# Optimization experiments

Measured on AMD Instinct MI355X. Metric: run time of the kernel, lower is better.

## Reference

```python
import jax, jax.numpy as jnp
import numpy as np

HEADS, DIM_HEAD, C, B, HS, WS = 8, 64, 512, 2, 48, 48


def setup_inputs() -> dict:
    key = jax.random.key(0)
    ks = jax.random.split(key, 9)
    s = 0.02
    return {
        "hidden_states": jax.random.normal(ks[0], (B, C, HS, WS), jnp.float32),
        "Wq": jax.random.normal(ks[1], (HEADS, DIM_HEAD, C), jnp.float32) * s,
        "bq": jax.random.normal(ks[2], (HEADS, DIM_HEAD), jnp.float32) * s,
        "Wk": jax.random.normal(ks[3], (HEADS, DIM_HEAD, C), jnp.float32) * s,
        "bk": jax.random.normal(ks[4], (HEADS, DIM_HEAD), jnp.float32) * s,
        "Wv": jax.random.normal(ks[5], (HEADS, DIM_HEAD, C), jnp.float32) * s,
        "bv": jax.random.normal(ks[6], (HEADS, DIM_HEAD), jnp.float32) * s,
        "Wo": jax.random.normal(ks[7], (C, HEADS * DIM_HEAD), jnp.float32) * s,
        "bo": jax.random.normal(ks[8], (C,), jnp.float32) * s,
    }


def reference(hidden_states, Wq, bq, Wk, bk, Wv, bv, Wo, bo):
    # hidden_states: [B, C, H, W]; per-head 1x1 convs == per-head linear over C.
    b, c, h, w = hidden_states.shape
    hw = h * w
    x = hidden_states.reshape(b, c, hw)  # [B, C, HW]
    # Batched per-head projections (fuses the per-head Conv2d loop).
    q = jnp.einsum('bcs,ndc->bnsd', x, Wq) + bq[None, :, None, :]  # [B, n, HW, d]
    k = jnp.einsum('bcs,ndc->bnsd', x, Wk) + bk[None, :, None, :]
    v = jnp.einsum('bcs,ndc->bnsd', x, Wv) + bv[None, :, None, :]
    scale = 1.0 / jnp.sqrt(jnp.asarray(DIM_HEAD, hidden_states.dtype))
    scores = jnp.einsum('bnqd,bnkd->bnqk', q, k) * scale  # [B, n, HW, HW]
    probs = jax.nn.softmax(scores, axis=-1)
    attn = jnp.einsum('bnqk,bnkd->bnqd', probs, v)  # [B, n, HW, d]
    # concat heads along last dim (matches torch.cat(..., dim=-1))
    attn = attn.transpose(0, 2, 1, 3).reshape(b, hw, HEADS * DIM_HEAD)
    out = attn @ Wo.T + bo  # [B, HW, C] (to_out[0]; to_out[1] dropout = identity)
    out = out.reshape(b, h, w, c).transpose(0, 3, 1, 2)  # [B, C, H, W]
    return out
```

## Files before the change

### kernel.cpp

```cpp
#include <hip/hip_runtime.h>
#include <hip/hip_bf16.h>

#define HEADS 8
#define DHEAD 64
#define CDIM  512
#define SEQ   2304
#define ND    512
#define NCHUNK 4

typedef unsigned short u16;
typedef unsigned int   u32;
typedef __attribute__((ext_vector_type(8))) short short8;
typedef __attribute__((ext_vector_type(4))) float f32x4;

#define QSCALE 0.18033688011112043f

__device__ __forceinline__ u16 f2bf(float f) {
    union { float f; u32 u; } x; x.f = f;
    u32 r = x.u + 0x7FFFu + ((x.u >> 16) & 1u);
    return (u16)(r >> 16);
}
__device__ __forceinline__ float bf2f(u16 v) {
    union { u32 u; float f; } x; x.u = ((u32)v) << 16; return x.f;
}
__device__ __forceinline__ u32 pkbf(float a, float b) {
    union { float f; u32 u; } x, y; x.f = a; y.f = b;
    return __builtin_amdgcn_perm(y.u + 0x8000u, x.u + 0x8000u, 0x07060302u);
}
__device__ __forceinline__ u32 cvtpk(float lo, float hi) {
    u32 r;
    asm("v_cvt_pk_bf16_f32 %0, %1, %2" : "=v"(r) : "v"(lo), "v"(hi));
    return r;
}
__device__ __forceinline__ f32x4 mfma16(short8 a, short8 b, f32x4 c) {
    return __builtin_amdgcn_mfma_f32_16x16x32_bf16(a, b, c, 0, 0, 0);
}
__device__ __forceinline__ void cp16(const void* g, void* l) {
    __builtin_amdgcn_global_load_lds(
        (const __attribute__((address_space(1))) u32*)(uintptr_t)g,
        (__attribute__((address_space(3))) u32*)(u32)(uintptr_t)l,
        16, 0, 0);
}
__device__ __forceinline__ int kperm_inv(int r) {
    return (r & ~0x1C) | ((r & 0x0C) << 1) | ((r & 0x10) >> 2);
}

__global__ void prep_kernel(const float* __restrict__ H,
                            const float* __restrict__ Wq, const float* __restrict__ Wk,
                            const float* __restrict__ Wv, const float* __restrict__ Wo,
                            u16* __restrict__ Wqkv, u16* __restrict__ Wob,
                            u16* __restrict__ X) {
    __shared__ float tile[32][33];
    const int t = threadIdx.x;
    const int bx = blockIdx.x;
    if (bx < 512) {
        const int N1 = CDIM * ND;
        int i8 = (bx * 256 + t) * 8;
        const float* src;
        u16* dst;
        if (i8 < 3 * N1) {
            src = (i8 < N1) ? &Wq[i8] : (i8 < 2 * N1 ? &Wk[i8 - N1] : &Wv[i8 - 2 * N1]);
            dst = &Wqkv[i8];
        } else {
            src = &Wo[i8 - 3 * N1];
            dst = &Wob[i8 - 3 * N1];
        }
        float4 a = *(const float4*)src;
        float4 c = *(const float4*)(src + 4);
        uint4 o;
        o.x = pkbf(a.x, a.y); o.y = pkbf(a.z, a.w);
        o.z = pkbf(c.x, c.y); o.w = pkbf(c.z, c.w);
        *(uint4*)dst = o;
    } else {
        int bb = bx - 512;
        int st = bb % 72, ct = (bb / 72) % 16, b = bb / (72 * 16);
        int cl = t >> 3, j4 = (t & 7) * 4;
        float4 hv = *(const float4*)&H[((size_t)b * CDIM + ct * 32 + cl) * SEQ + st * 32 + j4];
        tile[cl][j4 + 0] = hv.x; tile[cl][j4 + 1] = hv.y;
        tile[cl][j4 + 2] = hv.z; tile[cl][j4 + 3] = hv.w;
        __syncthreads();
        int sl = t >> 3, c4 = (t & 7) * 4;
        uint2 ov;
        ov.x = cvtpk(tile[c4 + 0][sl], tile[c4 + 1][sl]);
        ov.y = cvtpk(tile[c4 + 2][sl], tile[c4 + 3][sl]);
        *(uint2*)&X[((size_t)b * SEQ + st * 32 + sl) * CDIM + ct * 32 + c4] = ov;
    }
}

__global__ __launch_bounds__(256) void gemm_qkv_kernel(
        const u16* __restrict__ W, const u16* __restrict__ X,
        const float* __restrict__ bq, const float* __restrict__ bk, const float* __restrict__ bv,
        u16* __restrict__ Q, u16* __restrict__ K, u16* __restrict__ V) {
    __shared__ __align__(16) u16 sm[2 * (64 * 64 + 128 * 64)];
    const int n0 = blockIdx.x * 128;
    const int m0 = blockIdx.y * 64;
    const int b  = blockIdx.z;
    const int t = threadIdx.x;
    const int lane = t & 63, w = t >> 6;
    const int l16 = lane & 15, quad = lane >> 4;
    const int x7 = l16 & 7;
    const int srow = t >> 3, scol = (t & 7) * 8;
    const int scol_sw = ((t & 7) ^ (srow & 7)) * 8;
    const u16* Xb = X + (size_t)b * SEQ * CDIM;

    f32x4 acc[4][2] = {};

    {
        u16* As = sm; u16* Bs = sm + 4096;
#pragma unroll
        for (int it = 0; it < 2; ++it) {
            int r2 = it * 32 + srow;
            cp16(&W[(size_t)(m0 + r2) * 512 + scol_sw], &As[r2 * 64 + scol]);
        }
#pragma unroll
        for (int it = 0; it < 4; ++it) {
            int r2 = it * 32 + srow;
            cp16(&Xb[(size_t)(n0 + r2) * 512 + scol_sw], &Bs[r2 * 64 + scol]);
        }
    }
    for (int kb = 0; kb < 512; kb += 64) {
        const int pb = (kb >> 6) & 1;
        const u16* As = sm + pb * 12288;
        const u16* Bs = As + 4096;
        __syncthreads();
        if (kb + 64 < 512) {
            u16* An = sm + (pb ^ 1) * 12288;
            u16* Bn = An + 4096;
#pragma unroll
            for (int it = 0; it < 2; ++it) {
                int r2 = it * 32 + srow;
                cp16(&W[(size_t)(m0 + r2) * 512 + kb + 64 + scol_sw], &An[r2 * 64 + scol]);
            }
#pragma unroll
            for (int it = 0; it < 4; ++it) {
                int r2 = it * 32 + srow;
                cp16(&Xb[(size_t)(n0 + r2) * 512 + kb + 64 + scol_sw], &Bn[r2 * 64 + scol]);
            }
        }
#pragma unroll
        for (int kk = 0; kk < 2; ++kk) {
            const int co = ((kk * 4 + quad) ^ x7) * 8;
            short8 af[4], bfr[2];
#pragma unroll
            for (int i = 0; i < 4; ++i)
                af[i] = *(const short8*)&As[(i * 16 + l16) * 64 + co];
#pragma unroll
            for (int j = 0; j < 2; ++j)
                bfr[j] = *(const short8*)&Bs[(w * 32 + j * 16 + l16) * 64 + co];
#pragma unroll
            for (int i = 0; i < 4; ++i)
#pragma unroll
                for (int j = 0; j < 2; ++j)
                    acc[i][j] = mfma16(af[i], bfr[j], acc[i][j]);
        }
    }

    if (m0 < 1024) {
        const bool isQ = (m0 < 512);
        const float* bias = isQ ? bq : bk;
        const float sc = isQ ? QSCALE : 1.0f;
        const int mq = isQ ? m0 : m0 - 512;
        u16* dst = isQ ? Q : K;
#pragma unroll
        for (int j = 0; j < 2; ++j) {
            int s = n0 + w * 32 + j * 16 + l16;
#pragma unroll
            for (int i = 0; i < 4; ++i) {
                int mm = mq + i * 16 + quad * 4;
                uint2 val;
                val.x = pkbf((acc[i][j][0] + bias[mm + 0]) * sc, (acc[i][j][1] + bias[mm + 1]) * sc);
                val.y = pkbf((acc[i][j][2] + bias[mm + 2]) * sc, (acc[i][j][3] + bias[mm + 3]) * sc);
                *(uint2*)&dst[(((size_t)(b * 8 + (mm >> 6))) * SEQ + s) * 64 + (mm & 63)] = val;
            }
        }
    } else {
        __syncthreads();
        u16* vb = sm;
        const int mv = m0 - 1024;
#pragma unroll
        for (int j = 0; j < 2; ++j) {
            int sl = w * 32 + j * 16 + l16;
#pragma unroll
            for (int i = 0; i < 4; ++i) {
                int mb = i * 16 + quad * 4;
#pragma unroll
                for (int r = 0; r < 4; ++r)
                    vb[(mb + r) * 144 + sl] = f2bf(acc[i][j][r] + bv[mv + mb + r]);
            }
        }
        __syncthreads();
#pragma unroll
        for (int k2 = 0; k2 < 4; ++k2) {
            int v = k2 * 256 + t;
            int row = v >> 4, ch = (v & 15) * 8;
            *(uint4*)&V[((size_t)(b * 512 + mv + row)) * SEQ + n0 + ch] =
                *(const uint4*)&vb[row * 144 + ch];
        }
    }
}

__global__ __launch_bounds__(256, 3) void attn_partial(
        const u16* __restrict__ Q,
        const u16* __restrict__ K,
        const u16* __restrict__ Vt,
        u16* __restrict__ Opart,
        float* __restrict__ Lpart) {
    __shared__ __align__(16) u16 sm[2 * 8192];
    const int pair = blockIdx.x & 15, qt = blockIdx.x >> 4;
    const int c = blockIdx.y;
    const int b = pair >> 3, h = pair & 7;
    const int t = threadIdx.x, lane = t & 63, w = t >> 6;
    const int l16 = lane & 15, quad = lane >> 4;
    const int x7 = l16 & 7;
    const int srow = t >> 3;
    const int scol = (t & 7) * 8;
    const int scol_sw = ((t & 7) ^ (srow & 7)) * 8;
    const int kinv0 = kperm_inv(srow), kinv1 = kperm_inv(32 + srow);
    const int cA = (quad ^ x7) * 8;
    const int cB = (quad ^ x7 ^ 4) * 8;

    const u16* Qg = Q + ((size_t)pair * SEQ + qt * 192) * 64;
    const int rA = w * 16 + l16;
    short8 qf[3][2];
#pragma unroll
    for (int G = 0; G < 3; ++G) {
        qf[G][0] = *(const short8*)&Qg[(size_t)(G * 64 + rA) * 64 + quad * 8];
        qf[G][1] = *(const short8*)&Qg[(size_t)(G * 64 + rA) * 64 + 32 + quad * 8];
    }

    const u16* Kg = K  + ((size_t)pair * SEQ + c * 576) * 64;
    const u16* Vg = Vt + ((size_t)(b * 512 + h * 64)) * SEQ + c * 576;

    float lacc[3] = {0.f, 0.f, 0.f};
    f32x4 o[3][4] = {};

    {
        u16* Ks = sm; u16* Vs = sm + 4096;
        cp16(&Kg[(size_t)kinv0 * 64 + scol_sw], &Ks[srow * 64 + scol]);
        cp16(&Kg[(size_t)kinv1 * 64 + scol_sw], &Ks[(32 + srow) * 64 + scol]);
        cp16(&Vg[(size_t)srow * SEQ + scol_sw],        &Vs[srow * 64 + scol]);
        cp16(&Vg[(size_t)(32 + srow) * SEQ + scol_sw], &Vs[(32 + srow) * 64 + scol]);
    }
    for (int kt = 0; kt < 9; ++kt) {
        const int pb = kt & 1;
        const u16* Ks = sm + pb * 8192;
        const u16* Vs = Ks + 4096;
        __syncthreads();
        if (kt < 8) {
            u16* Kn = sm + (pb ^ 1) * 8192;
            u16* Vn = Kn + 4096;
            cp16(&Kg[(size_t)((kt + 1) * 64 + kinv0) * 64 + scol_sw], &Kn[srow * 64 + scol]);
            cp16(&Kg[(size_t)((kt + 1) * 64 + kinv1) * 64 + scol_sw], &Kn[(32 + srow) * 64 + scol]);
            cp16(&Vg[(size_t)srow * SEQ + (kt + 1) * 64 + scol_sw],        &Vn[srow * 64 + scol]);
            cp16(&Vg[(size_t)(32 + srow) * SEQ + (kt + 1) * 64 + scol_sw], &Vn[(32 + srow) * 64 + scol]);
        }
        f32x4 sacc[3][4];
        __builtin_amdgcn_s_setprio(1);
#pragma unroll
        for (int j = 0; j < 4; ++j) {
            short8 kf0 = *(const short8*)&Ks[(j * 16 + l16) * 64 + cA];
            short8 kf1 = *(const short8*)&Ks[(j * 16 + l16) * 64 + cB];
#pragma unroll
            for (int G = 0; G < 3; ++G) {
                f32x4 z = {0.f, 0.f, 0.f, 0.f};
                z = mfma16(kf0, qf[G][0], z);
                sacc[G][j] = mfma16(kf1, qf[G][1], z);
            }
        }
        __builtin_amdgcn_s_setprio(0);
        short8 pks[3][2];
#pragma unroll
        for (int G = 0; G < 3; ++G)
#pragma unroll
            for (int j = 0; j < 4; ++j) {
                float e0 = __builtin_amdgcn_exp2f(sacc[G][j][0]);
                float e1 = __builtin_amdgcn_exp2f(sacc[G][j][1]);
                float e2 = __builtin_amdgcn_exp2f(sacc[G][j][2]);
                float e3 = __builtin_amdgcn_exp2f(sacc[G][j][3]);
                lacc[G] += (e0 + e1) + (e2 + e3);
                u32* pw = (u32*)&pks[G][j >> 1];
                pw[(j & 1) * 2 + 0] = cvtpk(e0, e1);
                pw[(j & 1) * 2 + 1] = cvtpk(e2, e3);
            }
        __builtin_amdgcn_s_setprio(1);
#pragma unroll
        for (int g = 0; g < 2; ++g) {
            const int cg = g ? cB : cA;
#pragma unroll
            for (int i = 0; i < 4; ++i) {
                short8 vf = *(const short8*)&Vs[(i * 16 + l16) * 64 + cg];
#pragma unroll
                for (int G = 0; G < 3; ++G)
                    o[G][i] = mfma16(vf, pks[G][g], o[G][i]);
            }
        }
        __builtin_amdgcn_s_setprio(0);
    }
    float linv[3];
#pragma unroll
    for (int G = 0; G < 3; ++G) {
        float lr = lacc[G];
        lr += __shfl_xor(lr, 16);
        lr += __shfl_xor(lr, 32);
        if (quad == 0) Lpart[((size_t)(c * 16 + pair)) * SEQ + qt * 192 + G * 64 + rA] = lr;
        linv[G] = 1.0f / lr;
    }
    const size_t orow = ((size_t)(c * 16 + pair)) * SEQ + qt * 192;

    __syncthreads();
#pragma unroll
    for (int G = 0; G < 3; ++G)
#pragma unroll
        for (int i = 0; i < 4; ++i) {
            uint2 pkv;
            pkv.x = cvtpk(o[G][i][0] * linv[G], o[G][i][1] * linv[G]);
            pkv.y = cvtpk(o[G][i][2] * linv[G], o[G][i][3] * linv[G]);
            *(uint2*)&sm[(G * 64 + rA) * 72 + i * 16 + quad * 4] = pkv;
        }
    __syncthreads();
#pragma unroll
    for (int it = 0; it < 6; ++it) {
        int v = it * 256 + t;
        int row = v >> 3, col = (v & 7) * 8;
        *(uint4*)&Opart[(orow + row) * 64 + col] = *(const uint4*)&sm[row * 72 + col];
    }
}

__global__ __launch_bounds__(256) void attn_combine(
        const u16* __restrict__ Opart, const float* __restrict__ Lpart,
        u16* __restrict__ At) {
    const int bid = blockIdx.x;
    const int pair = bid / 72, sb = bid % 72;
    const int t = threadIdx.x;
    const int rl = t >> 3, dg = t & 7;
    const int s = sb * 32 + rl;
    const int b = pair >> 3, h = pair & 7;
    float wc[NCHUNK], L = 0.f;
#pragma unroll
    for (int c = 0; c < NCHUNK; ++c) {
        wc[c] = Lpart[(size_t)(c * 16 + pair) * SEQ + s];
        L += wc[c];
    }
    float invL = 1.0f / L;
    float acc[8] = {};
#pragma unroll
    for (int c = 0; c < NCHUNK; ++c) {
        uint4 v = *(const uint4*)&Opart[((size_t)(c * 16 + pair) * SEQ + s) * 64 + dg * 8];
        const u16* pv = (const u16*)&v;
#pragma unroll
        for (int e = 0; e < 8; ++e)
            acc[e] += wc[c] * bf2f(pv[e]);
    }
    uint4 outv;
    outv.x = pkbf(acc[0] * invL, acc[1] * invL);
    outv.y = pkbf(acc[2] * invL, acc[3] * invL);
    outv.z = pkbf(acc[4] * invL, acc[5] * invL);
    outv.w = pkbf(acc[6] * invL, acc[7] * invL);
    *(uint4*)&At[((size_t)b * SEQ + s) * ND + h * 64 + dg * 8] = outv;
}

__global__ __launch_bounds__(256) void gemm_out_kernel(
        const u16* __restrict__ Wob, const u16* __restrict__ At,
        const float* __restrict__ bo, float* __restrict__ out) {
    __shared__ __align__(16) u16 sm[2 * 8192];
    const int n0 = blockIdx.x * 64;
    const int m0 = blockIdx.y * 64;
    const int b  = blockIdx.z;
    const int t = threadIdx.x;
    const int lane = t & 63, w = t >> 6;
    const int l16 = lane & 15, quad = lane >> 4;
    const int x7 = l16 & 7;
    const int srow = t >> 3, scol = (t & 7) * 8;
    const int scol_sw = ((t & 7) ^ (srow & 7)) * 8;
    const u16* Ab = At + (size_t)b * SEQ * ND;

    f32x4 acc[4] = {};

    {
        u16* As = sm; u16* Bs = sm + 4096;
#pragma unroll
        for (int it = 0; it < 2; ++it) {
            int r2 = it * 32 + srow;
            cp16(&Wob[(size_t)(m0 + r2) * 512 + scol_sw], &As[r2 * 64 + scol]);
            cp16(&Ab [(size_t)(n0 + r2) * 512 + scol_sw], &Bs[r2 * 64 + scol]);
        }
    }
    for (int kb = 0; kb < 512; kb += 64) {
        const int pb = (kb >> 6) & 1;
        const u16* As = sm + pb * 8192;
        const u16* Bs = As + 4096;
        __syncthreads();
        if (kb + 64 < 512) {
            u16* An = sm + (pb ^ 1) * 8192;
            u16* Bn = An + 4096;
#pragma unroll
            for (int it = 0; it < 2; ++it) {
                int r2 = it * 32 + srow;
                cp16(&Wob[(size_t)(m0 + r2) * 512 + kb + 64 + scol_sw], &An[r2 * 64 + scol]);
                cp16(&Ab [(size_t)(n0 + r2) * 512 + kb + 64 + scol_sw], &Bn[r2 * 64 + scol]);
            }
        }
#pragma unroll
        for (int kk = 0; kk < 2; ++kk) {
            const int co = ((kk * 4 + quad) ^ x7) * 8;
            short8 af[4];
#pragma unroll
            for (int i = 0; i < 4; ++i)
                af[i] = *(const short8*)&As[(i * 16 + l16) * 64 + co];
            short8 bfr = *(const short8*)&Bs[(w * 16 + l16) * 64 + co];
#pragma unroll
            for (int i = 0; i < 4; ++i)
                acc[i] = mfma16(af[i], bfr, acc[i]);
        }
    }
    __syncthreads();
    float* fb = (float*)sm;
#pragma unroll
    for (int i = 0; i < 4; ++i) {
        int cl = i * 16 + quad * 4;
        int s = w * 16 + l16;
#pragma unroll
        for (int r = 0; r < 4; ++r)
            fb[(cl + r) * 68 + s] = acc[i][r] + bo[m0 + cl + r];
    }
    __syncthreads();
#pragma unroll
    for (int k2 = 0; k2 < 4; ++k2) {
        int v = k2 * 256 + t;
        int row = v >> 4, c4 = (v & 15) * 4;
        f32x4 ov = *(const f32x4*)&fb[row * 68 + c4];
        __builtin_nontemporal_store(ov, (f32x4*)&out[((size_t)(b * 512 + m0 + row)) * SEQ + n0 + c4]);
    }
}

extern "C" void kernel_launch(void* const* d_in, const int* in_sizes, int n_in,
                              void* d_out, int out_size, void* d_ws, size_t ws_size,
                              hipStream_t stream) {
    const float* H  = (const float*)d_in[0];
    const float* Wq = (const float*)d_in[1];
    const float* bq = (const float*)d_in[2];
    const float* Wk = (const float*)d_in[3];
    const float* bk = (const float*)d_in[4];
    const float* Wv = (const float*)d_in[5];
    const float* bv = (const float*)d_in[6];
    const float* Wo = (const float*)d_in[7];
    const float* bo = (const float*)d_in[8];
    float* out = (float*)d_out;

    u16* ws    = (u16*)d_ws;
    u16* Wqkv  = ws;
    u16* Wob   = Wqkv  + 1536 * 512;
    u16* Xbf   = Wob   + 512 * 512;
    u16* Qb    = Xbf   + 2 * SEQ * CDIM;
    u16* Kb    = Qb    + 2 * SEQ * ND;
    u16* Vb    = Kb    + 2 * SEQ * ND;
    u16* At    = Vb    + 2 * SEQ * ND;
    u16* Opart = At    + 2 * SEQ * ND;
    float* Lpart = (float*)(Opart + NCHUNK * 16 * SEQ * 64);

    prep_kernel<<<2816, 256, 0, stream>>>(H, Wq, Wk, Wv, Wo, Wqkv, Wob, Xbf);
    gemm_qkv_kernel<<<dim3(18, 24, 2), 256, 0, stream>>>(Wqkv, Xbf, bq, bk, bv, Qb, Kb, Vb);
    attn_partial<<<dim3(192, NCHUNK), 256, 0, stream>>>(Qb, Kb, Vb, Opart, Lpart);
    attn_combine<<<1152, 256, 0, stream>>>(Opart, Lpart, At);
    gemm_out_kernel<<<dim3(36, 8, 2), 256, 0, stream>>>(Wob, At, bo, out);
}
```

Before: 130.9 us.

## Enlarge QKV GEMM tile, stage Q/K stores via LDS, widen prep transpose tiles

The QKV projection GEMM now uses a 128x128 output tile instead of 64x128. Each block computes 8x2 MFMA accumulators per wave, halving the grid and improving reuse of the X tile. Q/K outputs are staged through shared memory so the global writes become coalesced 16-byte row stores instead of scattered 8-byte stores. The input transpose in prep_kernel uses 64x64 tiles with wider stores. The trade-offs are more LDS and register pressure (launch bounds set to 2 waves/SIMD) and fewer blocks, which lowers parallelism.

```diff
diff --git a/kernel.cpp b/kernel.cpp
--- a/kernel.cpp
+++ b/kernel.cpp
@@ -50,7 +50,7 @@
                             const float* __restrict__ Wv, const float* __restrict__ Wo,
                             u16* __restrict__ Wqkv, u16* __restrict__ Wob,
                             u16* __restrict__ X) {
-    __shared__ float tile[32][33];
+    __shared__ float tile[64][65];
     const int t = threadIdx.x;
     const int bx = blockIdx.x;
     if (bx < 512) {
@@ -73,27 +73,39 @@
         *(uint4*)dst = o;
     } else {
         int bb = bx - 512;
-        int st = bb % 72, ct = (bb / 72) % 16, b = bb / (72 * 16);
-        int cl = t >> 3, j4 = (t & 7) * 4;
-        float4 hv = *(const float4*)&H[((size_t)b * CDIM + ct * 32 + cl) * SEQ + st * 32 + j4];
-        tile[cl][j4 + 0] = hv.x; tile[cl][j4 + 1] = hv.y;
-        tile[cl][j4 + 2] = hv.z; tile[cl][j4 + 3] = hv.w;
-        __syncthreads();
-        int sl = t >> 3, c4 = (t & 7) * 4;
-        uint2 ov;
-        ov.x = cvtpk(tile[c4 + 0][sl], tile[c4 + 1][sl]);
-        ov.y = cvtpk(tile[c4 + 2][sl], tile[c4 + 3][sl]);
-        *(uint2*)&X[((size_t)b * SEQ + st * 32 + sl) * CDIM + ct * 32 + c4] = ov;
-    }
-}
-
-__global__ __launch_bounds__(256) void gemm_qkv_kernel(
+        int st = bb % 36, ct = (bb / 36) % 8, b = bb / (36 * 8);
+#pragma unroll
+        for (int it = 0; it < 4; ++it) {
+            int cl = it * 16 + (t >> 4);
+            int j4 = (t & 15) * 4;
+            float4 hv = *(const float4*)&H[((size_t)(b * CDIM + ct * 64 + cl)) * SEQ + st * 64 + j4];
+            tile[cl][j4 + 0] = hv.x; tile[cl][j4 + 1] = hv.y;
+            tile[cl][j4 + 2] = hv.z; tile[cl][j4 + 3] = hv.w;
+        }
+        __syncthreads();
+        int sl = t >> 2, c16 = (t & 3) * 16;
+        uint4 o1, o2;
+        o1.x = cvtpk(tile[c16 +  0][sl], tile[c16 +  1][sl]);
+        o1.y = cvtpk(tile[c16 +  2][sl], tile[c16 +  3][sl]);
+        o1.z = cvtpk(tile[c16 +  4][sl], tile[c16 +  5][sl]);
+        o1.w = cvtpk(tile[c16 +  6][sl], tile[c16 +  7][sl]);
+        o2.x = cvtpk(tile[c16 +  8][sl], tile[c16 +  9][sl]);
+        o2.y = cvtpk(tile[c16 + 10][sl], tile[c16 + 11][sl]);
+        o2.z = cvtpk(tile[c16 + 12][sl], tile[c16 + 13][sl]);
+        o2.w = cvtpk(tile[c16 + 14][sl], tile[c16 + 15][sl]);
+        u16* xp = &X[((size_t)(b * SEQ + st * 64 + sl)) * CDIM + ct * 64 + c16];
+        *(uint4*)xp = o1;
+        *(uint4*)(xp + 8) = o2;
+    }
+}
+
+__global__ __launch_bounds__(256, 2) void gemm_qkv_kernel(
         const u16* __restrict__ W, const u16* __restrict__ X,
         const float* __restrict__ bq, const float* __restrict__ bk, const float* __restrict__ bv,
         u16* __restrict__ Q, u16* __restrict__ K, u16* __restrict__ V) {
-    __shared__ __align__(16) u16 sm[2 * (64 * 64 + 128 * 64)];
+    __shared__ __align__(16) u16 sm[2 * (128 * 64 + 128 * 64)];
     const int n0 = blockIdx.x * 128;
-    const int m0 = blockIdx.y * 64;
+    const int m0 = blockIdx.y * 128;
     const int b  = blockIdx.z;
     const int t = threadIdx.x;
     const int lane = t & 63, w = t >> 6;
@@ -103,98 +115,101 @@
     const int scol_sw = ((t & 7) ^ (srow & 7)) * 8;
     const u16* Xb = X + (size_t)b * SEQ * CDIM;
 
-    f32x4 acc[4][2] = {};
+    f32x4 acc[8][2] = {};
 
     {
-        u16* As = sm; u16* Bs = sm + 4096;
-#pragma unroll
-        for (int it = 0; it < 2; ++it) {
-            int r2 = it * 32 + srow;
-            cp16(&W[(size_t)(m0 + r2) * 512 + scol_sw], &As[r2 * 64 + scol]);
-        }
+        u16* As = sm; u16* Bs = sm + 8192;
 #pragma unroll
         for (int it = 0; it < 4; ++it) {
             int r2 = it * 32 + srow;
+            cp16(&W [(size_t)(m0 + r2) * 512 + scol_sw], &As[r2 * 64 + scol]);
             cp16(&Xb[(size_t)(n0 + r2) * 512 + scol_sw], &Bs[r2 * 64 + scol]);
         }
     }
     for (int kb = 0; kb < 512; kb += 64) {
         const int pb = (kb >> 6) & 1;
-        const u16* As = sm + pb * 12288;
-        const u16* Bs = As + 4096;
+        const u16* As = sm + pb * 16384;
+        const u16* Bs = As + 8192;
         __syncthreads();
         if (kb + 64 < 512) {
-            u16* An = sm + (pb ^ 1) * 12288;
-            u16* Bn = An + 4096;
-#pragma unroll
-            for (int it = 0; it < 2; ++it) {
-                int r2 = it * 32 + srow;
-                cp16(&W[(size_t)(m0 + r2) * 512 + kb + 64 + scol_sw], &An[r2 * 64 + scol]);
-            }
+            u16* An = sm + (pb ^ 1) * 16384;
+            u16* Bn = An + 8192;
 #pragma unroll
             for (int it = 0; it < 4; ++it) {
                 int r2 = it * 32 + srow;
+                cp16(&W [(size_t)(m0 + r2) * 512 + kb + 64 + scol_sw], &An[r2 * 64 + scol]);
                 cp16(&Xb[(size_t)(n0 + r2) * 512 + kb + 64 + scol_sw], &Bn[r2 * 64 + scol]);
             }
         }
 #pragma unroll
         for (int kk = 0; kk < 2; ++kk) {
             const int co = ((kk * 4 + quad) ^ x7) * 8;
-            short8 af[4], bfr[2];
-#pragma unroll
-            for (int i = 0; i < 4; ++i)
-                af[i] = *(const short8*)&As[(i * 16 + l16) * 64 + co];
+            short8 af[8], bfr[2];
 #pragma unroll
             for (int j = 0; j < 2; ++j)
                 bfr[j] = *(const short8*)&Bs[(w * 32 + j * 16 + l16) * 64 + co];
 #pragma unroll
-            for (int i = 0; i < 4; ++i)
+            for (int i = 0; i < 8; ++i)
+                af[i] = *(const short8*)&As[(i * 16 + l16) * 64 + co];
+#pragma unroll
+            for (int i = 0; i < 8; ++i)
 #pragma unroll
                 for (int j = 0; j < 2; ++j)
                     acc[i][j] = mfma16(af[i], bfr[j], acc[i][j]);
         }
     }
 
+    __syncthreads();
     if (m0 < 1024) {
         const bool isQ = (m0 < 512);
         const float* bias = isQ ? bq : bk;
         const float sc = isQ ? QSCALE : 1.0f;
         const int mq = isQ ? m0 : m0 - 512;
         u16* dst = isQ ? Q : K;
+        u16* qb = sm;
 #pragma unroll
         for (int j = 0; j < 2; ++j) {
-            int s = n0 + w * 32 + j * 16 + l16;
-#pragma unroll
-            for (int i = 0; i < 4; ++i) {
-                int mm = mq + i * 16 + quad * 4;
+            int sl = w * 32 + j * 16 + l16;
+#pragma unroll
+            for (int i = 0; i < 8; ++i) {
+                int md = i * 16 + quad * 4;
+                int mm = mq + md;
                 uint2 val;
                 val.x = pkbf((acc[i][j][0] + bias[mm + 0]) * sc, (acc[i][j][1] + bias[mm + 1]) * sc);
                 val.y = pkbf((acc[i][j][2] + bias[mm + 2]) * sc, (acc[i][j][3] + bias[mm + 3]) * sc);
-                *(uint2*)&dst[(((size_t)(b * 8 + (mm >> 6))) * SEQ + s) * 64 + (mm & 63)] = val;
-            }
+                *(uint2*)&qb[sl * 136 + md] = val;
+            }
+        }
+        __syncthreads();
+#pragma unroll
+        for (int it = 0; it < 8; ++it) {
+            int v = it * 256 + t;
+            int row = v >> 4, c8 = (v & 15) * 8;
+            int hh = mq + c8;
+            *(uint4*)&dst[(((size_t)(b * 8 + (hh >> 6))) * SEQ + n0 + row) * 64 + (hh & 63)] =
+                *(const uint4*)&qb[row * 136 + c8];
         }
     } else {
-        __syncthreads();
         u16* vb = sm;
         const int mv = m0 - 1024;
 #pragma unroll
         for (int j = 0; j < 2; ++j) {
             int sl = w * 32 + j * 16 + l16;
 #pragma unroll
-            for (int i = 0; i < 4; ++i) {
+            for (int i = 0; i < 8; ++i) {
                 int mb = i * 16 + quad * 4;
 #pragma unroll
                 for (int r = 0; r < 4; ++r)
-                    vb[(mb + r) * 144 + sl] = f2bf(acc[i][j][r] + bv[mv + mb + r]);
-            }
-        }
-        __syncthreads();
-#pragma unroll
-        for (int k2 = 0; k2 < 4; ++k2) {
-            int v = k2 * 256 + t;
+                    vb[(mb + r) * 136 + sl] = f2bf(acc[i][j][r] + bv[mv + mb + r]);
+            }
+        }
+        __syncthreads();
+#pragma unroll
+        for (int it = 0; it < 8; ++it) {
+            int v = it * 256 + t;
             int row = v >> 4, ch = (v & 15) * 8;
             *(uint4*)&V[((size_t)(b * 512 + mv + row)) * SEQ + n0 + ch] =
-                *(const uint4*)&vb[row * 144 + ch];
+                *(const uint4*)&vb[row * 136 + ch];
         }
     }
 }
@@ -458,8 +473,8 @@
     u16* Opart = At    + 2 * SEQ * ND;
     float* Lpart = (float*)(Opart + NCHUNK * 16 * SEQ * 64);
 
-    prep_kernel<<<2816, 256, 0, stream>>>(H, Wq, Wk, Wv, Wo, Wqkv, Wob, Xbf);
-    gemm_qkv_kernel<<<dim3(18, 24, 2), 256, 0, stream>>>(Wqkv, Xbf, bq, bk, bv, Qb, Kb, Vb);
+    prep_kernel<<<1088, 256, 0, stream>>>(H, Wq, Wk, Wv, Wo, Wqkv, Wob, Xbf);
+    gemm_qkv_kernel<<<dim3(18, 12, 2), 256, 0, stream>>>(Wqkv, Xbf, bq, bk, bv, Qb, Kb, Vb);
     attn_partial<<<dim3(192, NCHUNK), 256, 0, stream>>>(Qb, Kb, Vb, Opart, Lpart);
     attn_combine<<<1152, 256, 0, stream>>>(Opart, Lpart, At);
     gemm_out_kernel<<<dim3(36, 8, 2), 256, 0, stream>>>(Wob, At, bo, out);
```

New measurement: 128.3 us, median of 2. 1.02x faster.
